# Performance work log

Hardware: AMD Instinct MI355X
Metric: run time of the kernel (lower is better)

## Reference

```python
import jax, jax.numpy as jnp
import numpy as np

N = 100000   # total nodes
E = 1000000  # edges
D = 64       # input_dim
H = 128      # embed_dim


def setup_inputs() -> dict:
    key = jax.random.key(0)
    k1, k2, k3, k4 = jax.random.split(key, 4)
    nodes = jnp.arange(N, dtype=jnp.int32)
    features = jax.random.normal(k1, (N, D), dtype=jnp.float32)
    edge_index = jax.random.randint(k2, (2, E), 0, N, dtype=jnp.int32)
    # nn.Linear(2*D, H): weight [H, 2D], bias [H]
    W = jax.random.normal(k3, (H, 2 * D), dtype=jnp.float32) / np.sqrt(2 * D)
    b = jax.random.normal(k4, (H,), dtype=jnp.float32) * 0.01
    return {"nodes": nodes, "features": features, "edge_index": edge_index,
            "W": W, "b": b}


def reference(nodes, features, edge_index, W, b):
    src, dst = edge_index[0], edge_index[1]
    # gcn=False: neighbors are undirected (both src->dst and dst->src).
    # Mean aggregator over all neighbors (full-neighborhood mean).
    ones = jnp.ones((E,), dtype=features.dtype)
    neigh_sum = (jax.ops.segment_sum(features[dst], src, num_segments=N)
                 + jax.ops.segment_sum(features[src], dst, num_segments=N))
    deg = (jax.ops.segment_sum(ones, src, num_segments=N)
           + jax.ops.segment_sum(ones, dst, num_segments=N))
    neigh_mean = neigh_sum / jnp.maximum(deg, 1.0)[:, None]  # [N, D]
    self_feats = features[nodes]            # [B, D]
    neigh_feats = neigh_mean[nodes]         # [B, D]
    combined = jnp.concatenate([self_feats, neigh_feats], axis=1)  # [B, 2D]
    out = jax.nn.relu(combined @ W.T + b)   # [B, H]
    return out
```

## Files before the change

### kernel.cpp

```cpp
#include <hip/hip_runtime.h>
#include <hip/hip_bf16.h>


#define D_IN 64
#define H_OUT 128
#define CAP 64
#define CAP_L 61
#define NPB 32
#define BSHIFT 8
#define BUK_N 256
#define NBUK_MAX 512
#define PASSA_BLOCKS 256
#define PASSA_THREADS 512

typedef unsigned long long ull;
typedef unsigned short ushortt;
typedef unsigned char uchar;
typedef __attribute__((ext_vector_type(8))) short bf16x8;
typedef __attribute__((ext_vector_type(4))) float f32x4;
typedef __attribute__((ext_vector_type(2))) float f32x2;

__device__ __forceinline__ ushortt f2bf(float f) {
    __hip_bfloat16 h = __float2bfloat16(f);
    return *reinterpret_cast<ushortt*>(&h);
}
__device__ __forceinline__ float bf2f(ushortt u) {
    unsigned int x = ((unsigned int)u) << 16;
    return __uint_as_float(x);
}

__global__ __launch_bounds__(PASSA_THREADS) void prep_kernel(
    const int* __restrict__ ei,
    unsigned* __restrict__ gbuf,
    int* __restrict__ blkcnt,
    const float4* __restrict__ feat4,
    const float4* __restrict__ w4,
    ushortt* __restrict__ fb,
    uint2* __restrict__ fq,
    ushortt* __restrict__ Wb,
    int E, int nbuk, int scap, int chunk, int nfeat8, int nw8)
{
    const int t = threadIdx.x;

    if (blockIdx.x >= PASSA_BLOCKS) {
        int i = (blockIdx.x - PASSA_BLOCKS) * PASSA_THREADS + t;
        if (i < nfeat8) {
            float4 a = feat4[2 * i], b = feat4[2 * i + 1];
            bf16x8 o;
            o[0] = (short)f2bf(a.x); o[1] = (short)f2bf(a.y);
            o[2] = (short)f2bf(a.z); o[3] = (short)f2bf(a.w);
            o[4] = (short)f2bf(b.x); o[5] = (short)f2bf(b.y);
            o[6] = (short)f2bf(b.z); o[7] = (short)f2bf(b.w);
            *(bf16x8*)&fb[(size_t)i * 8] = o;
            unsigned lo = (unsigned)__builtin_amdgcn_cvt_pk_fp8_f32(a.x, a.y, 0, false);
            lo = (unsigned)__builtin_amdgcn_cvt_pk_fp8_f32(a.z, a.w, (int)lo, true);
            unsigned hi = (unsigned)__builtin_amdgcn_cvt_pk_fp8_f32(b.x, b.y, 0, false);
            hi = (unsigned)__builtin_amdgcn_cvt_pk_fp8_f32(b.z, b.w, (int)hi, true);
            uint2 q; q.x = lo; q.y = hi;
            fq[i] = q;
        } else {
            int j = i - nfeat8;
            if (j < nw8) {
                float4 a = w4[2 * j], b = w4[2 * j + 1];
                bf16x8 o;
                o[0] = (short)f2bf(a.x); o[1] = (short)f2bf(a.y);
                o[2] = (short)f2bf(a.z); o[3] = (short)f2bf(a.w);
                o[4] = (short)f2bf(b.x); o[5] = (short)f2bf(b.y);
                o[6] = (short)f2bf(b.z); o[7] = (short)f2bf(b.w);
                *(bf16x8*)&Wb[(size_t)j * 8] = o;
            }
        }
        return;
    }

    __shared__ int lcnt[NBUK_MAX];
    for (int i = t; i < nbuk; i += PASSA_THREADS) lcnt[i] = 0;
    __syncthreads();

    const int E2 = 2 * E;
    int lo = blockIdx.x * chunk;
    int hi = lo + chunk; if (hi > E2) hi = E2;

    for (int i = lo + t; i < hi; i += PASSA_THREADS) {
        int u = ei[i];
        int v = (i < E) ? ei[E + i] : ei[i - E];
        int b = u >> BSHIFT;
        unsigned pk = ((unsigned)v << BSHIFT) | (unsigned)(u & (BUK_N - 1));
        int p = atomicAdd(&lcnt[b], 1);
        if (p < scap) gbuf[((size_t)blockIdx.x * nbuk + b) * scap + p] = pk;
    }
    __syncthreads();
    for (int b = t; b < nbuk; b += PASSA_THREADS)
        blkcnt[blockIdx.x * nbuk + b] = lcnt[b];
}

__global__ __launch_bounds__(1024) void adj_agg_kernel(
    const unsigned* __restrict__ gbuf,
    const int* __restrict__ blkcnt,
    const int* __restrict__ ei,
    const uchar* __restrict__ fq,
    ushortt* __restrict__ meanb,
    int N, int E, int nbuk, int scap)
{
    __shared__ unsigned adj_l[BUK_N * CAP_L];
    __shared__ int cnt_l[BUK_N];
    __shared__ int scnt_l[PASSA_BLOCKS];
    __shared__ int satf;

    const int b = blockIdx.x;
    const int t = threadIdx.x;

    if (t == 0) satf = 0;
    if (t < BUK_N) cnt_l[t] = 0;
    if (t < PASSA_BLOCKS) {
        int c = blkcnt[t * nbuk + b];
        scnt_l[t] = c;
        if (c > scap) satf = 1;
    }
    __syncthreads();

    const int wv   = t >> 6;
    const int lane = t & 63;

    if (satf) {
        const int E2 = 2 * E;
        for (int i = t; i < E2; i += 1024) {
            int u = ei[i];
            if ((u >> BSHIFT) != b) continue;
            int v = (i < E) ? ei[E + i] : ei[i - E];
            int ul = u & (BUK_N - 1);
            int p  = atomicAdd(&cnt_l[ul], 1);
            if (p < CAP_L) adj_l[ul * CAP_L + p] = (unsigned)v;
        }
    } else {
        for (int seg = wv; seg < PASSA_BLOCKS; seg += 16) {
            int c = scnt_l[seg]; if (c > scap) c = scap;
            const unsigned* base = gbuf + ((size_t)seg * nbuk + b) * scap;
            for (int i = lane; i < c; i += 64) {
                unsigned e = base[i];
                int ul = e & (BUK_N - 1);
                int v  = (int)(e >> BSHIFT);
                int p  = atomicAdd(&cnt_l[ul], 1);
                if (p < CAP_L) adj_l[ul * CAP_L + p] = (unsigned)v;
            }
        }
    }
    __syncthreads();

    const int oct = lane >> 3;
    const int ol  = lane & 7;
    const uchar* fqb = fq + ol * 8;

    for (int ni = 0; ni < 16; ++ni) {
        const int n = wv * 16 + ni;
        const int g = (b << BSHIFT) + n;
        if (g >= N) break;

        const int c  = cnt_l[n];
        const int cc = c < CAP_L ? c : CAP_L;
        const unsigned* arow = &adj_l[n * CAP_L];

        uint2 u0 = {0u, 0u}, u1 = {0u, 0u}, u2 = {0u, 0u}, u3 = {0u, 0u};
        if (cc > 0) {
            int jj = oct;      int a = jj < cc;
            unsigned id = arow[a ? jj : 0];
            u0 = *(const uint2*)(fqb + (size_t)(id * 64u));
            if (!a) { u0.x = 0u; u0.y = 0u; }
        }
        if (cc > 8) {
            int jj = 8 + oct;  int a = jj < cc;
            unsigned id = arow[a ? jj : 0];
            u1 = *(const uint2*)(fqb + (size_t)(id * 64u));
            if (!a) { u1.x = 0u; u1.y = 0u; }
        }
        if (cc > 16) {
            int jj = 16 + oct; int a = jj < cc;
            unsigned id = arow[a ? jj : 0];
            u2 = *(const uint2*)(fqb + (size_t)(id * 64u));
            if (!a) { u2.x = 0u; u2.y = 0u; }
        }
        if (cc > 24) {
            int jj = 24 + oct; int a = jj < cc;
            unsigned id = arow[a ? jj : 0];
            u3 = *(const uint2*)(fqb + (size_t)(id * 64u));
            if (!a) { u3.x = 0u; u3.y = 0u; }
        }

        f32x2 s0 = {0.f, 0.f}, s1 = {0.f, 0.f}, s2 = {0.f, 0.f}, s3 = {0.f, 0.f};
#define DEC(u)                                                       \
        s0 += __builtin_amdgcn_cvt_pk_f32_fp8((int)(u).x, false);    \
        s1 += __builtin_amdgcn_cvt_pk_f32_fp8((int)(u).x, true);     \
        s2 += __builtin_amdgcn_cvt_pk_f32_fp8((int)(u).y, false);    \
        s3 += __builtin_amdgcn_cvt_pk_f32_fp8((int)(u).y, true);
        DEC(u0); DEC(u1); DEC(u2); DEC(u3);

        if (__builtin_expect(cc > 32, 0)) {
            for (int j = 32; j < cc; j += 8) {
                int jj = j + oct; int a = jj < cc;
                unsigned id = arow[a ? jj : 0];
                uint2 u = *(const uint2*)(fqb + (size_t)(id * 64u));
                if (!a) { u.x = 0u; u.y = 0u; }
                DEC(u);
            }
        }
#undef DEC

        f32x2 a0, a1;
        {
            f32x2 t0, t1, t2, t3;
            t0.x = __shfl_xor(s0.x, 8);  t0.y = __shfl_xor(s0.y, 8);
            t1.x = __shfl_xor(s1.x, 8);  t1.y = __shfl_xor(s1.y, 8);
            t2.x = __shfl_xor(s2.x, 8);  t2.y = __shfl_xor(s2.y, 8);
            t3.x = __shfl_xor(s3.x, 8);  t3.y = __shfl_xor(s3.y, 8);
            bool hi = (oct & 1);
            a0 = hi ? (s2 + t2) : (s0 + t0);
            a1 = hi ? (s3 + t3) : (s1 + t1);
        }
        f32x2 b0;
        {
            f32x2 t0, t1;
            t0.x = __shfl_xor(a0.x, 16); t0.y = __shfl_xor(a0.y, 16);
            t1.x = __shfl_xor(a1.x, 16); t1.y = __shfl_xor(a1.y, 16);
            bool hi = (oct & 2);
            b0 = hi ? (a1 + t1) : (a0 + t0);
        }
        float cf;
        {
            f32x2 tt; tt.x = __shfl_xor(b0.x, 32); tt.y = __shfl_xor(b0.y, 32);
            f32x2 ss = b0 + tt;
            cf = (oct & 4) ? ss.y : ss.x;
        }

        float r = 1.0f / fmaxf((float)c, 1.0f);
        int d = 8 * ol + 4 * (oct & 1) + (oct & 2) + ((oct >> 2) & 1);
        meanb[(size_t)g * D_IN + d] = f2bf(cf * r);
    }
}

__global__ __launch_bounds__(256) void build_adj_kernel(
    const int* __restrict__ ei,
    int* __restrict__ cnt,
    int* __restrict__ adj,
    int E)
{
    const int part   = blockIdx.x & 7;
    const int bloc   = blockIdx.x >> 3;
    const int nbp    = gridDim.x >> 3;
    const int stride = nbp * 256;
    const int E2     = 2 * E;

    for (int i = bloc * 256 + (int)threadIdx.x; i < E2; i += stride) {
        int u = ei[i];
        if (((u >> 4) & 7) != part) continue;
        int v = (i < E) ? ei[E + i] : ei[i - E];
        int p = atomicAdd(&cnt[u], 1);
        if (p < CAP_L) adj[u * CAP + p] = v;
    }
}

__global__ __launch_bounds__(256) void aggregate_f32_kernel(
    const float* __restrict__ feat,
    const int* __restrict__ adj,
    const int* __restrict__ cnt,
    ushortt* __restrict__ meanb,
    int N)
{
    int wid  = (blockIdx.x * blockDim.x + threadIdx.x) >> 6;
    int lane = threadIdx.x & 63;
    if (wid >= N) return;

    int c  = cnt[wid];
    int cc = c < CAP_L ? c : CAP_L;
    int ids = adj[wid * CAP + lane];

    float sum = 0.0f;
    int j = 0;
    for (; j + 8 <= cc; j += 8) {
        int i0 = __shfl(ids, j + 0);
        int i1 = __shfl(ids, j + 1);
        int i2 = __shfl(ids, j + 2);
        int i3 = __shfl(ids, j + 3);
        int i4 = __shfl(ids, j + 4);
        int i5 = __shfl(ids, j + 5);
        int i6 = __shfl(ids, j + 6);
        int i7 = __shfl(ids, j + 7);
        float f0 = feat[i0 * D_IN + lane];
        float f1 = feat[i1 * D_IN + lane];
        float f2 = feat[i2 * D_IN + lane];
        float f3 = feat[i3 * D_IN + lane];
        float f4 = feat[i4 * D_IN + lane];
        float f5 = feat[i5 * D_IN + lane];
        float f6 = feat[i6 * D_IN + lane];
        float f7 = feat[i7 * D_IN + lane];
        sum += ((f0 + f1) + (f2 + f3)) + ((f4 + f5) + (f6 + f7));
    }
    for (; j < cc; ++j)
        sum += feat[__shfl(ids, j) * D_IN + lane];

    float m = sum / fmaxf((float)c, 1.0f);
    meanb[(size_t)wid * D_IN + lane] = f2bf(m);
}

__global__ __launch_bounds__(256) void gemm_mfma_kernel(
    const int* __restrict__ nodes,
    const ushortt* __restrict__ fb,
    const ushortt* __restrict__ meanb,
    const ushortt* __restrict__ Wb,
    const float* __restrict__ bias,
    float* __restrict__ out,
    int N)
{
    __shared__ ushortt w_lds[128 * 136];
    __shared__ int gnode[64];

    const int t  = threadIdx.x;
    const int n0 = blockIdx.x * 64;

    if (t < 64) {
        int idx = n0 + t;
        gnode[t] = nodes[idx < N ? idx : N - 1];
    }
    for (int i = t; i < 128 * 16; i += 256) {
        int row = i >> 4, seg = i & 15;
        *(bf16x8*)&w_lds[row * 136 + seg * 8] =
            *(const bf16x8*)&Wb[row * 128 + seg * 8];
    }
    __syncthreads();

    const int w    = t >> 6;
    const int lane = t & 63;
    const int l15  = lane & 15;
    const int quad = lane >> 4;

    const int g = gnode[w * 16 + l15];
    const bf16x8 a0 = *(const bf16x8*)&fb[(size_t)g * D_IN +  0 + quad * 8];
    const bf16x8 a1 = *(const bf16x8*)&fb[(size_t)g * D_IN + 32 + quad * 8];
    const bf16x8 a2 = *(const bf16x8*)&meanb[(size_t)g * D_IN +  0 + quad * 8];
    const bf16x8 a3 = *(const bf16x8*)&meanb[(size_t)g * D_IN + 32 + quad * 8];

    const int  out_row = n0 + w * 16 + l15;
    const bool valid   = out_row < N;

#pragma unroll
    for (int tile = 0; tile < 8; ++tile) {
        const int h0 = tile * 16;
        const ushortt* wrow = &w_lds[(h0 + l15) * 136];
        bf16x8 b0 = *(const bf16x8*)&wrow[ 0 + quad * 8];
        bf16x8 b1 = *(const bf16x8*)&wrow[32 + quad * 8];
        bf16x8 b2 = *(const bf16x8*)&wrow[64 + quad * 8];
        bf16x8 b3 = *(const bf16x8*)&wrow[96 + quad * 8];

        f32x4 acc = {0.f, 0.f, 0.f, 0.f};
        acc = __builtin_amdgcn_mfma_f32_16x16x32_bf16(b0, a0, acc, 0, 0, 0);
        acc = __builtin_amdgcn_mfma_f32_16x16x32_bf16(b1, a1, acc, 0, 0, 0);
        acc = __builtin_amdgcn_mfma_f32_16x16x32_bf16(b2, a2, acc, 0, 0, 0);
        acc = __builtin_amdgcn_mfma_f32_16x16x32_bf16(b3, a3, acc, 0, 0, 0);

        if (valid) {
            float4 bv = *(const float4*)&bias[h0 + quad * 4];
            float4 o;
            o.x = fmaxf(acc[0] + bv.x, 0.0f);
            o.y = fmaxf(acc[1] + bv.y, 0.0f);
            o.z = fmaxf(acc[2] + bv.z, 0.0f);
            o.w = fmaxf(acc[3] + bv.w, 0.0f);
            *(float4*)&out[(size_t)out_row * H_OUT + h0 + quad * 4] = o;
        }
    }
}

__global__ __launch_bounds__(256) void gemm_kernel(
    const int* __restrict__ nodes,
    const float* __restrict__ feat,
    const ushortt* __restrict__ meanb,
    const float* __restrict__ W,
    const float* __restrict__ bias,
    float* __restrict__ out,
    int N)
{
    __shared__ float w_lds[64 * 132];
    __shared__ float comb_self[NPB * 68];
    __shared__ float comb_mean[NPB * 68];
    __shared__ int   gnode[NPB];

    const int t  = threadIdx.x;
    const int n0 = blockIdx.x * NPB;

    if (t < NPB) {
        int idx = n0 + t;
        if (idx >= N) idx = N - 1;
        gnode[t] = nodes[idx];
    }
    __syncthreads();

    for (int i = t; i < NPB * 64; i += 256) {
        int n = i >> 6, d = i & 63;
        int g = gnode[n];
        comb_self[n * 68 + d] = feat[g * D_IN + d];
        comb_mean[n * 68 + d] = bf2f(meanb[(size_t)g * D_IN + d]);
    }
    for (int i = t; i < H_OUT * 64; i += 256) {
        int h = i >> 6, kk = i & 63;
        w_lds[kk * 132 + h] = W[h * (2 * D_IN) + kk];
    }
    __syncthreads();

    const int tx = t & 31;
    const int ty = t >> 5;
    const int h0 = tx * 4;
    const int nl = ty * 4;

    float acc[4][4];
#pragma unroll
    for (int j = 0; j < 4; j++)
#pragma unroll
        for (int i = 0; i < 4; i++) acc[j][i] = 0.0f;

    for (int kk = 0; kk < 64; kk += 4) {
        float4 wvv[4], cv[4];
#pragma unroll
        for (int i = 0; i < 4; i++)
            wvv[i] = *(const float4*)&w_lds[(kk + i) * 132 + h0];
#pragma unroll
        for (int j = 0; j < 4; j++)
            cv[j] = *(const float4*)&comb_self[(nl + j) * 68 + kk];
#pragma unroll
        for (int j = 0; j < 4; j++) {
            const float* c = (const float*)&cv[j];
#pragma unroll
            for (int i = 0; i < 4; i++) {
                const float* wp = (const float*)&wvv[i];
                acc[j][0] += wp[0] * c[i];
                acc[j][1] += wp[1] * c[i];
                acc[j][2] += wp[2] * c[i];
                acc[j][3] += wp[3] * c[i];
            }
        }
    }
    __syncthreads();

    for (int i = t; i < H_OUT * 64; i += 256) {
        int h = i >> 6, kk = i & 63;
        w_lds[kk * 132 + h] = W[h * (2 * D_IN) + 64 + kk];
    }
    __syncthreads();

    for (int kk = 0; kk < 64; kk += 4) {
        float4 wvv[4], cv[4];
#pragma unroll
        for (int i = 0; i < 4; i++)
            wvv[i] = *(const float4*)&w_lds[(kk + i) * 132 + h0];
#pragma unroll
        for (int j = 0; j < 4; j++)
            cv[j] = *(const float4*)&comb_mean[(nl + j) * 68 + kk];
#pragma unroll
        for (int j = 0; j < 4; j++) {
            const float* c = (const float*)&cv[j];
#pragma unroll
            for (int i = 0; i < 4; i++) {
                const float* wp = (const float*)&wvv[i];
                acc[j][0] += wp[0] * c[i];
                acc[j][1] += wp[1] * c[i];
                acc[j][2] += wp[2] * c[i];
                acc[j][3] += wp[3] * c[i];
            }
        }
    }

    float4 bv = *(const float4*)&bias[h0];
#pragma unroll
    for (int j = 0; j < 4; j++) {
        int n = n0 + nl + j;
        if (n >= N) continue;
        float4 o;
        o.x = fmaxf(acc[j][0] + bv.x, 0.0f);
        o.y = fmaxf(acc[j][1] + bv.y, 0.0f);
        o.z = fmaxf(acc[j][2] + bv.z, 0.0f);
        o.w = fmaxf(acc[j][3] + bv.w, 0.0f);
        *(float4*)&out[(size_t)n * H_OUT + h0] = o;
    }
}

extern "C" void kernel_launch(void* const* d_in, const int* in_sizes, int n_in,
                              void* d_out, int out_size, void* d_ws, size_t ws_size,
                              hipStream_t stream) {
    const int*   nodes = (const int*)d_in[0];
    const float* feat  = (const float*)d_in[1];
    const int*   ei    = (const int*)d_in[2];
    const float* W     = (const float*)d_in[3];
    const float* bias  = (const float*)d_in[4];
    float*       out   = (float*)d_out;

    const int N  = in_sizes[0];
    const int E  = in_sizes[2] / 2;
    const int E2 = 2 * E;

    const int nbuk  = (N + BUK_N - 1) >> BSHIFT;
    const int chunk = (E2 + PASSA_BLOCKS - 1) / PASSA_BLOCKS;
    double ex = (double)chunk * (double)BUK_N / (double)N;
    int scap = ((int)(ex + 9.0 * __builtin_sqrt(ex)) + 31) & ~15;
    if (scap < 64) scap = 64;

    char* base = (char*)d_ws;
    size_t off = 0;
    auto aln = [](size_t x) { return (x + 63) & ~(size_t)63; };
    int*     cnt    = (int*)(base + off);     off = aln(off + (size_t)N * 4);
    int*     adj    = (int*)(base + off);     off = aln(off + (size_t)N * CAP * 4);
    ushortt* meanb  = (ushortt*)(base + off); off = aln(off + (size_t)N * D_IN * 2);
    int*     blkcnt = (int*)(base + off);     off = aln(off + (size_t)PASSA_BLOCKS * NBUK_MAX * 4);
    ushortt* Wb     = (ushortt*)(base + off); off = aln(off + (size_t)H_OUT * 2 * D_IN * 2);
    ushortt* fb     = (ushortt*)(base + off); off = aln(off + (size_t)N * D_IN * 2);
    uchar*   fq     = (uchar*)(base + off);   off = aln(off + (size_t)N * D_IN);
    unsigned* gbuf  = (unsigned*)(base + off);
    const size_t total = off + (size_t)PASSA_BLOCKS * nbuk * scap * 4;

    const bool full = (N <= 131072) && (nbuk <= NBUK_MAX) && (ws_size >= total)
                   && ((N * D_IN) % 8 == 0);

    if (full) {
        const int nfeat8 = N * D_IN / 8;
        const int nw8    = H_OUT * 2 * D_IN / 8;
        const int conv_blocks = (nfeat8 + nw8 + PASSA_THREADS - 1) / PASSA_THREADS;
        prep_kernel<<<PASSA_BLOCKS + conv_blocks, PASSA_THREADS, 0, stream>>>(
            ei, gbuf, blkcnt, (const float4*)feat, (const float4*)W,
            fb, (uint2*)fq, Wb, E, nbuk, scap, chunk, nfeat8, nw8);
        adj_agg_kernel<<<nbuk, 1024, 0, stream>>>(gbuf, blkcnt, ei, fq,
                                                  meanb, N, E, nbuk, scap);
        gemm_mfma_kernel<<<(N + 63) / 64, 256, 0, stream>>>(
            nodes, fb, meanb, Wb, bias, out, N);
    } else {
        const int ablocks = (int)(((size_t)N * 64 + 255) / 256);
        hipMemsetAsync(cnt, 0, (size_t)N * sizeof(int), stream);
        build_adj_kernel<<<2048, 256, 0, stream>>>(ei, cnt, adj, E);
        aggregate_f32_kernel<<<ablocks, 256, 0, stream>>>(feat, adj, cnt,
                                                          meanb, N);
        gemm_kernel<<<(N + NPB - 1) / NPB, 256, 0, stream>>>(
            nodes, feat, meanb, W, bias, out, N);
    }
}
```

Before: 169.6 us.

## Halve aggregation buckets and software-pipeline neighbor feature gathers

```diff
diff --git a/kernel.cpp b/kernel.cpp
--- a/kernel.cpp
+++ b/kernel.cpp
@@ -7,9 +7,9 @@
 #define CAP 64
 #define CAP_L 61
 #define NPB 32
-#define BSHIFT 8
-#define BUK_N 256
-#define NBUK_MAX 512
+#define BSHIFT 7
+#define BUK_N 128
+#define NBUK_MAX 1024
 #define PASSA_BLOCKS 256
 #define PASSA_THREADS 512
 
@@ -94,7 +94,7 @@
         blkcnt[blockIdx.x * nbuk + b] = lcnt[b];
 }
 
-__global__ __launch_bounds__(1024) void adj_agg_kernel(
+__global__ __launch_bounds__(512, 8) void adj_agg_kernel(
     const unsigned* __restrict__ gbuf,
     const int* __restrict__ blkcnt,
     const int* __restrict__ ei,
@@ -124,7 +124,7 @@
 
     if (satf) {
         const int E2 = 2 * E;
-        for (int i = t; i < E2; i += 1024) {
+        for (int i = t; i < E2; i += 512) {
             int u = ei[i];
             if ((u >> BSHIFT) != b) continue;
             int v = (i < E) ? ei[E + i] : ei[i - E];
@@ -133,7 +133,7 @@
             if (p < CAP_L) adj_l[ul * CAP_L + p] = (unsigned)v;
         }
     } else {
-        for (int seg = wv; seg < PASSA_BLOCKS; seg += 16) {
+        for (int seg = wv; seg < PASSA_BLOCKS; seg += 8) {
             int c = scnt_l[seg]; if (c > scap) c = scap;
             const unsigned* base = gbuf + ((size_t)seg * nbuk + b) * scap;
             for (int i = lane; i < c; i += 64) {
@@ -151,90 +151,119 @@
     const int ol  = lane & 7;
     const uchar* fqb = fq + ol * 8;
 
+    const int nbase = wv * 16;
+    const int gbase = (b << BSHIFT) + nbase;
+
+#define GATHER(U0, U1, U2, U3, AROW, CC)                                     \
+    {                                                                        \
+        if ((CC) > 0) {                                                      \
+            int jj = oct;      int a = jj < (CC);                            \
+            unsigned id = (AROW)[a ? jj : 0];                                \
+            U0 = *(const uint2*)(fqb + (size_t)(id * 64u));                  \
+            if (!a) { U0.x = 0u; U0.y = 0u; }                                \
+        } else { U0.x = 0u; U0.y = 0u; }                                     \
+        if ((CC) > 8) {                                                      \
+            int jj = 8 + oct;  int a = jj < (CC);                            \
+            unsigned id = (AROW)[a ? jj : 0];                                \
+            U1 = *(const uint2*)(fqb + (size_t)(id * 64u));                  \
+            if (!a) { U1.x = 0u; U1.y = 0u; }                                \
+        } else { U1.x = 0u; U1.y = 0u; }                                     \
+        if ((CC) > 16) {                                                     \
+            int jj = 16 + oct; int a = jj < (CC);                            \
+            unsigned id = (AROW)[a ? jj : 0];                                \
+            U2 = *(const uint2*)(fqb + (size_t)(id * 64u));                  \
+            if (!a) { U2.x = 0u; U2.y = 0u; }                                \
+        } else { U2.x = 0u; U2.y = 0u; }                                     \
+        if ((CC) > 24) {                                                     \
+            int jj = 24 + oct; int a = jj < (CC);                            \
+            unsigned id = (AROW)[a ? jj : 0];                                \
+            U3 = *(const uint2*)(fqb + (size_t)(id * 64u));                  \
+            if (!a) { U3.x = 0u; U3.y = 0u; }                                \
+        } else { U3.x = 0u; U3.y = 0u; }                                     \
+    }
+
+#define DEC(u)                                                       \
+    s0 += __builtin_amdgcn_cvt_pk_f32_fp8((int)(u).x, false);        \
+    s1 += __builtin_amdgcn_cvt_pk_f32_fp8((int)(u).x, true);         \
+    s2 += __builtin_amdgcn_cvt_pk_f32_fp8((int)(u).y, false);        \
+    s3 += __builtin_amdgcn_cvt_pk_f32_fp8((int)(u).y, true);
+
+    uint2 cu0, cu1, cu2, cu3;
+    uint2 nu0, nu1, nu2, nu3;
+
+    int c_cur = 0, cc_cur = 0;
+    {
+        if (gbase < N) c_cur = cnt_l[nbase];
+        cc_cur = c_cur < CAP_L ? c_cur : CAP_L;
+        const unsigned* arow = &adj_l[nbase * CAP_L];
+        GATHER(cu0, cu1, cu2, cu3, arow, cc_cur);
+    }
+
     for (int ni = 0; ni < 16; ++ni) {
-        const int n = wv * 16 + ni;
-        const int g = (b << BSHIFT) + n;
-        if (g >= N) break;
-
-        const int c  = cnt_l[n];
-        const int cc = c < CAP_L ? c : CAP_L;
-        const unsigned* arow = &adj_l[n * CAP_L];
-
-        uint2 u0 = {0u, 0u}, u1 = {0u, 0u}, u2 = {0u, 0u}, u3 = {0u, 0u};
-        if (cc > 0) {
-            int jj = oct;      int a = jj < cc;
-            unsigned id = arow[a ? jj : 0];
-            u0 = *(const uint2*)(fqb + (size_t)(id * 64u));
-            if (!a) { u0.x = 0u; u0.y = 0u; }
-        }
-        if (cc > 8) {
-            int jj = 8 + oct;  int a = jj < cc;
-            unsigned id = arow[a ? jj : 0];
-            u1 = *(const uint2*)(fqb + (size_t)(id * 64u));
-            if (!a) { u1.x = 0u; u1.y = 0u; }
-        }
-        if (cc > 16) {
-            int jj = 16 + oct; int a = jj < cc;
-            unsigned id = arow[a ? jj : 0];
-            u2 = *(const uint2*)(fqb + (size_t)(id * 64u));
-            if (!a) { u2.x = 0u; u2.y = 0u; }
-        }
-        if (cc > 24) {
-            int jj = 24 + oct; int a = jj < cc;
-            unsigned id = arow[a ? jj : 0];
-            u3 = *(const uint2*)(fqb + (size_t)(id * 64u));
-            if (!a) { u3.x = 0u; u3.y = 0u; }
-        }
-
-        f32x2 s0 = {0.f, 0.f}, s1 = {0.f, 0.f}, s2 = {0.f, 0.f}, s3 = {0.f, 0.f};
-#define DEC(u)                                                       \
-        s0 += __builtin_amdgcn_cvt_pk_f32_fp8((int)(u).x, false);    \
-        s1 += __builtin_amdgcn_cvt_pk_f32_fp8((int)(u).x, true);     \
-        s2 += __builtin_amdgcn_cvt_pk_f32_fp8((int)(u).y, false);    \
-        s3 += __builtin_amdgcn_cvt_pk_f32_fp8((int)(u).y, true);
-        DEC(u0); DEC(u1); DEC(u2); DEC(u3);
-
-        if (__builtin_expect(cc > 32, 0)) {
-            for (int j = 32; j < cc; j += 8) {
-                int jj = j + oct; int a = jj < cc;
-                unsigned id = arow[a ? jj : 0];
-                uint2 u = *(const uint2*)(fqb + (size_t)(id * 64u));
-                if (!a) { u.x = 0u; u.y = 0u; }
-                DEC(u);
-            }
-        }
+        const int n = nbase + ni;
+        const int g = gbase + ni;
+
+        int c_nxt = 0, cc_nxt = 0;
+        if (ni < 15) {
+            if (g + 1 < N) c_nxt = cnt_l[n + 1];
+            cc_nxt = c_nxt < CAP_L ? c_nxt : CAP_L;
+            const unsigned* arown = &adj_l[(n + 1) * CAP_L];
+            GATHER(nu0, nu1, nu2, nu3, arown, cc_nxt);
+        }
+
+        if (g < N) {
+            f32x2 s0 = {0.f, 0.f}, s1 = {0.f, 0.f};
+            f32x2 s2 = {0.f, 0.f}, s3 = {0.f, 0.f};
+            DEC(cu0); DEC(cu1); DEC(cu2); DEC(cu3);
+
+            if (__builtin_expect(cc_cur > 32, 0)) {
+                const unsigned* arow = &adj_l[n * CAP_L];
+                for (int j = 32; j < cc_cur; j += 8) {
+                    int jj = j + oct; int a = jj < cc_cur;
+                    unsigned id = arow[a ? jj : 0];
+                    uint2 u = *(const uint2*)(fqb + (size_t)(id * 64u));
+                    if (!a) { u.x = 0u; u.y = 0u; }
+                    DEC(u);
+                }
+            }
+
+            f32x2 a0, a1;
+            {
+                f32x2 t0, t1, t2, t3;
+                t0.x = __shfl_xor(s0.x, 8);  t0.y = __shfl_xor(s0.y, 8);
+                t1.x = __shfl_xor(s1.x, 8);  t1.y = __shfl_xor(s1.y, 8);
+                t2.x = __shfl_xor(s2.x, 8);  t2.y = __shfl_xor(s2.y, 8);
+                t3.x = __shfl_xor(s3.x, 8);  t3.y = __shfl_xor(s3.y, 8);
+                bool hi = (oct & 1);
+                a0 = hi ? (s2 + t2) : (s0 + t0);
+                a1 = hi ? (s3 + t3) : (s1 + t1);
+            }
+            f32x2 b0;
+            {
+                f32x2 t0, t1;
+                t0.x = __shfl_xor(a0.x, 16); t0.y = __shfl_xor(a0.y, 16);
+                t1.x = __shfl_xor(a1.x, 16); t1.y = __shfl_xor(a1.y, 16);
+                bool hi = (oct & 2);
+                b0 = hi ? (a1 + t1) : (a0 + t0);
+            }
+            float cf;
+            {
+                f32x2 tt;
+                tt.x = __shfl_xor(b0.x, 32); tt.y = __shfl_xor(b0.y, 32);
+                f32x2 ss = b0 + tt;
+                cf = (oct & 4) ? ss.y : ss.x;
+            }
+
+            float r = 1.0f / fmaxf((float)c_cur, 1.0f);
+            int d = 8 * ol + 4 * (oct & 1) + (oct & 2) + ((oct >> 2) & 1);
+            meanb[(size_t)g * D_IN + d] = f2bf(cf * r);
+        }
+
+        c_cur = c_nxt; cc_cur = cc_nxt;
+        cu0 = nu0; cu1 = nu1; cu2 = nu2; cu3 = nu3;
+    }
+#undef GATHER
 #undef DEC
-
-        f32x2 a0, a1;
-        {
-            f32x2 t0, t1, t2, t3;
-            t0.x = __shfl_xor(s0.x, 8);  t0.y = __shfl_xor(s0.y, 8);
-            t1.x = __shfl_xor(s1.x, 8);  t1.y = __shfl_xor(s1.y, 8);
-            t2.x = __shfl_xor(s2.x, 8);  t2.y = __shfl_xor(s2.y, 8);
-            t3.x = __shfl_xor(s3.x, 8);  t3.y = __shfl_xor(s3.y, 8);
-            bool hi = (oct & 1);
-            a0 = hi ? (s2 + t2) : (s0 + t0);
-            a1 = hi ? (s3 + t3) : (s1 + t1);
-        }
-        f32x2 b0;
-        {
-            f32x2 t0, t1;
-            t0.x = __shfl_xor(a0.x, 16); t0.y = __shfl_xor(a0.y, 16);
-            t1.x = __shfl_xor(a1.x, 16); t1.y = __shfl_xor(a1.y, 16);
-            bool hi = (oct & 2);
-            b0 = hi ? (a1 + t1) : (a0 + t0);
-        }
-        float cf;
-        {
-            f32x2 tt; tt.x = __shfl_xor(b0.x, 32); tt.y = __shfl_xor(b0.y, 32);
-            f32x2 ss = b0 + tt;
-            cf = (oct & 4) ? ss.y : ss.x;
-        }
-
-        float r = 1.0f / fmaxf((float)c, 1.0f);
-        int d = 8 * ol + 4 * (oct & 1) + (oct & 2) + ((oct >> 2) & 1);
-        meanb[(size_t)g * D_IN + d] = f2bf(cf * r);
-    }
 }
 
 __global__ __launch_bounds__(256) void build_adj_kernel(
@@ -523,8 +552,8 @@
         prep_kernel<<<PASSA_BLOCKS + conv_blocks, PASSA_THREADS, 0, stream>>>(
             ei, gbuf, blkcnt, (const float4*)feat, (const float4*)W,
             fb, (uint2*)fq, Wb, E, nbuk, scap, chunk, nfeat8, nw8);
-        adj_agg_kernel<<<nbuk, 1024, 0, stream>>>(gbuf, blkcnt, ei, fq,
-                                                  meanb, N, E, nbuk, scap);
+        adj_agg_kernel<<<nbuk, 512, 0, stream>>>(gbuf, blkcnt, ei, fq,
+                                                 meanb, N, E, nbuk, scap);
         gemm_mfma_kernel<<<(N + 63) / 64, 256, 0, stream>>>(
             nodes, fb, meanb, Wb, bias, out, N);
     } else {
```

Measured after the change: 192.3 us. 13.4% more time.
